# Kernel tuning notes

Hardware: AMD Instinct MI355X
Metric: run time of the kernel (lower is better)

## Reference

```python
import jax, jax.numpy as jnp
import numpy as np

B, T, H, NH = 2, 2048, 1024, 16
D = H // NH          # head dim = 64
K_CONV = 4           # short conv kernel size


def _dwconv_silu(x, w):
    # causal depthwise conv1d + silu; x:[B,T,C], w:[C,K]
    Kc = w.shape[1]
    xp = jnp.pad(x, ((0, 0), (Kc - 1, 0), (0, 0))).transpose(0, 2, 1)  # [B,C,T+K-1]
    y = jax.lax.conv_general_dilated(xp, w[:, None, :], (1,), 'VALID',
                                     feature_group_count=w.shape[0],
                                     dimension_numbers=('NCH', 'OIH', 'NCH'))
    return jax.nn.silu(y.transpose(0, 2, 1))


def _l2norm(x, eps=1e-6):
    return x * jax.lax.rsqrt(jnp.sum(x * x, -1, keepdims=True) + eps)


def _forward(hidden, Wq, Wk, Wv, conv_q, conv_k, conv_v, Wb, Wa, A_log, dt_bias, Wg, norm_w, Wo):
    Bh, Tt, Hh = hidden.shape
    nh = A_log.shape[0]
    d = Hh // nh
    q = _dwconv_silu(hidden @ Wq.T, conv_q).reshape(Bh, Tt, nh, d)
    k = _dwconv_silu(hidden @ Wk.T, conv_k).reshape(Bh, Tt, nh, d)
    v = _dwconv_silu(hidden @ Wv.T, conv_v).reshape(Bh, Tt, nh, d)
    q = _l2norm(q) * (d ** -0.5)
    k = _l2norm(k)
    beta = jax.nn.sigmoid(hidden @ Wb.T)                                  # [B,T,h]
    g = -jnp.exp(A_log) * jax.nn.softplus(hidden @ Wa.T + dt_bias)        # [B,T,h]

    def step(S, inp):
        qt, kt, vt, gt, bt = inp
        S = S * jnp.exp(gt)[..., None, None]                 # gated decay
        pred = jnp.einsum('bhk,bhkv->bhv', kt, S)            # current memory readout
        dv = (vt - pred) * bt[..., None]                     # delta-rule update
        S = S + jnp.einsum('bhk,bhv->bhkv', kt, dv)
        ot = jnp.einsum('bhk,bhkv->bhv', qt, S)
        return S, ot

    xs = (q.transpose(1, 0, 2, 3), k.transpose(1, 0, 2, 3), v.transpose(1, 0, 2, 3),
          g.transpose(1, 0, 2), beta.transpose(1, 0, 2))
    S0 = jnp.zeros((Bh, nh, d, d), hidden.dtype)
    _, o = jax.lax.scan(step, S0, xs)
    o = o.transpose(1, 0, 2, 3)                               # [B,T,h,d]
    gate = (hidden @ Wg.T).reshape(Bh, Tt, nh, d)
    o = o * jax.lax.rsqrt(jnp.mean(o * o, -1, keepdims=True) + 1e-5) * norm_w
    o = o * jax.nn.silu(gate)                                 # gated RMSNorm
    return o.reshape(Bh, Tt, Hh) @ Wo.T


def setup_inputs():
    key = jax.random.key(0)
    ks = jax.random.split(key, 16)
    s = 0.02
    return {
        'hidden': jax.random.normal(ks[0], (B, T, H), jnp.float32),
        'Wq': jax.random.normal(ks[1], (H, H), jnp.float32) * s,
        'Wk': jax.random.normal(ks[2], (H, H), jnp.float32) * s,
        'Wv': jax.random.normal(ks[3], (H, H), jnp.float32) * s,
        'conv_q': jax.random.normal(ks[4], (H, K_CONV), jnp.float32) * 0.5,
        'conv_k': jax.random.normal(ks[5], (H, K_CONV), jnp.float32) * 0.5,
        'conv_v': jax.random.normal(ks[6], (H, K_CONV), jnp.float32) * 0.5,
        'Wb': jax.random.normal(ks[7], (NH, H), jnp.float32) * s,
        'Wa': jax.random.normal(ks[8], (NH, H), jnp.float32) * s,
        'A_log': jnp.log(jax.random.uniform(ks[9], (NH,), jnp.float32, 1.0, 16.0)),
        'dt_bias': jnp.log(jnp.expm1(jax.random.uniform(ks[10], (NH,), jnp.float32, 1e-3, 0.1))),
        'Wg': jax.random.normal(ks[11], (H, H), jnp.float32) * s,
        'norm_w': jnp.ones((D,), jnp.float32),
        'Wo': jax.random.normal(ks[12], (H, H), jnp.float32) * s,
    }


def reference(hidden, Wq, Wk, Wv, conv_q, conv_k, conv_v, Wb, Wa, A_log, dt_bias, Wg, norm_w, Wo):
    return _forward(hidden, Wq, Wk, Wv, conv_q, conv_k, conv_v, Wb, Wa, A_log, dt_bias, Wg, norm_w, Wo)
```

## Files before the change

### kernel.cpp

```cpp
#include <hip/hip_runtime.h>
#include <hip/hip_bf16.h>

typedef unsigned short u16;
typedef __attribute__((ext_vector_type(4))) float f32x4;
typedef __attribute__((ext_vector_type(8))) short bf16x8;

#define TLEN 2048
#define NHEAD 16
#define HD 1024

__device__ inline u16 f2bf(float f) {
  unsigned x = __float_as_uint(f);
  return (u16)((x + 0x7fffu + ((x >> 16) & 1u)) >> 16);
}
__device__ inline float bf2f(u16 u) { return __uint_as_float(((unsigned)u) << 16); }

__device__ inline unsigned pkbf(float lo, float hi) {
  unsigned r;
  asm("v_cvt_pk_bf16_f32 %0, %1, %2" : "=v"(r) : "v"(lo), "v"(hi));
  return r;
}

__device__ inline void storev(float* p, float v) { *p = v; }
__device__ inline void storev(u16* p, float v)   { *p = f2bf(v); }

__device__ inline int rowx(int row) { return (row ^ (row >> 3)) & 7; }
__device__ inline int swz(int row, int col) {
  return (row << 7) + (((col >> 3) ^ rowx(row)) << 4) + ((col & 7) << 1);
}
__device__ inline bf16x8 frag(const u16* base, int row, int kslot) {
  return *(const bf16x8*)((const char*)base + (row << 7) +
                          ((kslot ^ rowx(row)) << 4));
}

__global__ __launch_bounds__(256) void cvt_all(
    const float* __restrict__ h,  const float* __restrict__ wq,
    const float* __restrict__ wk, const float* __restrict__ wv,
    const float* __restrict__ wg, const float* __restrict__ wo,
    const float* __restrict__ Wb, const float* __restrict__ Wa,
    u16* __restrict__ dh,  u16* __restrict__ dhlo,
    u16* __restrict__ dwq, u16* __restrict__ dwk,
    u16* __restrict__ dwv, u16* __restrict__ dwg, u16* __restrict__ dwo,
    u16* __restrict__ dwba_h, u16* __restrict__ dwba_l) {
  const int b = blockIdx.x;
  if (b < 4096) {
    const size_t i = (size_t)b * 256 + threadIdx.x;
    float4 v = *(const float4*)(h + i * 4);
    ushort4 hi, lo;
    hi.x = f2bf(v.x); lo.x = f2bf(v.x - bf2f(hi.x));
    hi.y = f2bf(v.y); lo.y = f2bf(v.y - bf2f(hi.y));
    hi.z = f2bf(v.z); lo.z = f2bf(v.z - bf2f(hi.z));
    hi.w = f2bf(v.w); lo.w = f2bf(v.w - bf2f(hi.w));
    *(ushort4*)(dh + i * 4) = hi;
    *(ushort4*)(dhlo + i * 4) = lo;
  } else if (b < 9216) {
    const int wsel = (b - 4096) >> 10;
    const size_t i = (size_t)((b - 4096) & 1023) * 256 + threadIdx.x;
    const float* s; u16* d;
    switch (wsel) {
      case 0: s = wq; d = dwq; break;
      case 1: s = wk; d = dwk; break;
      case 2: s = wv; d = dwv; break;
      case 3: s = wg; d = dwg; break;
      default: s = wo; d = dwo; break;
    }
    float4 v = *(const float4*)(s + i * 4);
    ushort4 u;
    u.x = f2bf(v.x); u.y = f2bf(v.y); u.z = f2bf(v.z); u.w = f2bf(v.w);
    *(ushort4*)(d + i * 4) = u;
  } else {
    const size_t i = (size_t)(b - 9216) * 256 + threadIdx.x;
    const size_t flat = i * 4;
    const float* src = (flat < 16384) ? (Wb + flat) : (Wa + (flat - 16384));
    float4 v = *(const float4*)src;
    ushort4 hi, lo;
    hi.x = f2bf(v.x); lo.x = f2bf(v.x - bf2f(hi.x));
    hi.y = f2bf(v.y); lo.y = f2bf(v.y - bf2f(hi.y));
    hi.z = f2bf(v.z); lo.z = f2bf(v.z - bf2f(hi.z));
    hi.w = f2bf(v.w); lo.w = f2bf(v.w - bf2f(hi.w));
    *(ushort4*)(dwba_h + flat) = hi;
    *(ushort4*)(dwba_l + flat) = lo;
  }
}

__global__ __launch_bounds__(256, 2) void gemm_big(
    const u16* __restrict__ A,
    const u16* __restrict__ W0p, const u16* __restrict__ W1p,
    const u16* __restrict__ W2p, const u16* __restrict__ W3p,
    u16* __restrict__ C0, u16* __restrict__ C1,
    u16* __restrict__ C2, u16* __restrict__ C3,
    int M, int N, int K) {
  const u16* W; u16* C;
  switch (blockIdx.z) {
    case 0: W = W0p; C = C0; break;
    case 1: W = W1p; C = C1; break;
    case 2: W = W2p; C = C2; break;
    default: W = W3p; C = C3; break;
  }
  const int tid = threadIdx.x;
  const int lane = tid & 63, wid = tid >> 6;
  const int fr = lane & 15, fq = lane >> 4;
  const int row0 = blockIdx.y * 256, col0 = blockIdx.x * 128;
  __shared__ __align__(16) u16 As[256 * 64];
  __shared__ __align__(16) u16 Bs[128 * 64];

  const u16* aSrc[8]; const u16* bSrc[4];
#pragma unroll
  for (int it = 0; it < 8; ++it) {
    const int s = it * 256 + tid;
    const int r = s >> 3, cc = s & 7;
    aSrc[it] = A + (size_t)(row0 + r) * K + (cc ^ (r & 7)) * 8;
  }
#pragma unroll
  for (int it = 0; it < 4; ++it) {
    const int s = it * 256 + tid;
    const int r = s >> 3, cc = s & 7;
    bSrc[it] = W + (size_t)(col0 + r) * K + (cc ^ (r & 7)) * 8;
  }
  int aOff[4][2], bOff[8][2];
#pragma unroll
  for (int m = 0; m < 4; ++m)
#pragma unroll
    for (int kk = 0; kk < 2; ++kk) {
      const int ra = wid * 64 + m * 16 + fr;
      aOff[m][kk] = ra * 128 + ((((kk << 2) | fq) ^ (ra & 7)) << 4);
    }
#pragma unroll
  for (int n = 0; n < 8; ++n)
#pragma unroll
    for (int kk = 0; kk < 2; ++kk) {
      const int rb = n * 16 + fr;
      bOff[n][kk] = rb * 128 + ((((kk << 2) | fq) ^ (rb & 7)) << 4);
    }

  f32x4 acc[4][8] = {};
  for (int k0 = 0; k0 < K; k0 += 64) {
#pragma unroll
    for (int it = 0; it < 8; ++it)
      __builtin_amdgcn_global_load_lds(
          (const __attribute__((address_space(1))) void*)(aSrc[it] + k0),
          (__attribute__((address_space(3))) void*)((char*)As + (it * 256 + tid) * 16),
          16, 0, 0);
#pragma unroll
    for (int it = 0; it < 4; ++it)
      __builtin_amdgcn_global_load_lds(
          (const __attribute__((address_space(1))) void*)(bSrc[it] + k0),
          (__attribute__((address_space(3))) void*)((char*)Bs + (it * 256 + tid) * 16),
          16, 0, 0);
    __syncthreads();
#pragma unroll
    for (int kk = 0; kk < 2; ++kk) {
      bf16x8 af[4], bfr[8];
#pragma unroll
      for (int m = 0; m < 4; ++m)
        af[m] = *(const bf16x8*)((const char*)As + aOff[m][kk]);
#pragma unroll
      for (int n = 0; n < 8; ++n)
        bfr[n] = *(const bf16x8*)((const char*)Bs + bOff[n][kk]);
#pragma unroll
      for (int m = 0; m < 4; ++m)
#pragma unroll
        for (int n = 0; n < 8; ++n)
          acc[m][n] = __builtin_amdgcn_mfma_f32_16x16x32_bf16(af[m], bfr[n], acc[m][n], 0, 0, 0);
    }
    __syncthreads();
  }
#pragma unroll
  for (int m = 0; m < 4; ++m)
#pragma unroll
    for (int n = 0; n < 8; ++n) {
      const int gr0 = row0 + wid * 64 + m * 16 + fq * 4;
      const int gc = col0 + n * 16 + fr;
      const unsigned c01 = pkbf(acc[m][n][0], acc[m][n][1]);
      const unsigned c23 = pkbf(acc[m][n][2], acc[m][n][3]);
      C[(size_t)(gr0 + 0) * N + gc] = (u16)c01;
      C[(size_t)(gr0 + 1) * N + gc] = (u16)(c01 >> 16);
      C[(size_t)(gr0 + 2) * N + gc] = (u16)c23;
      C[(size_t)(gr0 + 3) * N + gc] = (u16)(c23 >> 16);
    }
}

template <typename OutT, int MT>
__global__ __launch_bounds__(256) void gemm_lin(
    const u16* __restrict__ A, const u16* __restrict__ W,
    OutT* __restrict__ C, int M, int N, int K) {
  const int tid = threadIdx.x;
  const int lane = tid & 63, wid = tid >> 6;
  const int wr = wid >> 1, wc = wid & 1;
  const int fr = lane & 15, fq = lane >> 4;
  const int row0 = blockIdx.y * (MT * 32), col0 = blockIdx.x * 128;
  __shared__ __align__(16) u16 As[MT * 32 * 64];
  __shared__ __align__(16) u16 Bs[128 * 64];

  const u16* aSrc[MT]; const u16* bSrc[4];
#pragma unroll
  for (int it = 0; it < MT; ++it) {
    const int c = it * 256 + tid;
    const int r = c >> 3, cc = c & 7, sc = cc ^ (r & 7);
    aSrc[it] = A + (size_t)(row0 + r) * K + sc * 8;
  }
#pragma unroll
  for (int it = 0; it < 4; ++it) {
    const int c = it * 256 + tid;
    const int r = c >> 3, cc = c & 7, sc = cc ^ (r & 7);
    bSrc[it] = W + (size_t)(col0 + r) * K + sc * 8;
  }
  int aOff[MT][2], bOff[4][2];
#pragma unroll
  for (int m = 0; m < MT; ++m)
#pragma unroll
    for (int kk = 0; kk < 2; ++kk) {
      const int ra = wr * (MT * 16) + m * 16 + fr;
      aOff[m][kk] = ra * 128 + ((((kk << 2) | fq) ^ (fr & 7)) << 4);
    }
#pragma unroll
  for (int n = 0; n < 4; ++n)
#pragma unroll
    for (int kk = 0; kk < 2; ++kk) {
      const int rb = wc * 64 + n * 16 + fr;
      bOff[n][kk] = rb * 128 + ((((kk << 2) | fq) ^ (fr & 7)) << 4);
    }

  f32x4 acc[MT][4] = {};
  for (int k0 = 0; k0 < K; k0 += 64) {
#pragma unroll
    for (int it = 0; it < MT; ++it)
      __builtin_amdgcn_global_load_lds(
          (const __attribute__((address_space(1))) void*)(aSrc[it] + k0),
          (__attribute__((address_space(3))) void*)((char*)As + (it * 256 + wid * 64) * 16),
          16, 0, 0);
#pragma unroll
    for (int it = 0; it < 4; ++it)
      __builtin_amdgcn_global_load_lds(
          (const __attribute__((address_space(1))) void*)(bSrc[it] + k0),
          (__attribute__((address_space(3))) void*)((char*)Bs + (it * 256 + wid * 64) * 16),
          16, 0, 0);
    __syncthreads();
#pragma unroll
    for (int kk = 0; kk < 2; ++kk) {
      bf16x8 af[MT], bfr[4];
#pragma unroll
      for (int m = 0; m < MT; ++m)
        af[m] = *(const bf16x8*)((const char*)As + aOff[m][kk]);
#pragma unroll
      for (int n = 0; n < 4; ++n)
        bfr[n] = *(const bf16x8*)((const char*)Bs + bOff[n][kk]);
#pragma unroll
      for (int m = 0; m < MT; ++m)
#pragma unroll
        for (int n = 0; n < 4; ++n)
          acc[m][n] = __builtin_amdgcn_mfma_f32_16x16x32_bf16(af[m], bfr[n], acc[m][n], 0, 0, 0);
    }
    __syncthreads();
  }
#pragma unroll
  for (int m = 0; m < MT; ++m)
#pragma unroll
    for (int n = 0; n < 4; ++n)
#pragma unroll
      for (int r = 0; r < 4; ++r) {
        const int gr = row0 + wr * (MT * 16) + m * 16 + fq * 4 + r;
        const int gc = col0 + wc * 64 + n * 16 + fr;
        storev(&C[(size_t)gr * N + gc], acc[m][n][r]);
      }
}

__global__ __launch_bounds__(256) void small_mfma(
    const u16* __restrict__ hhi, const u16* __restrict__ hlo,
    const u16* __restrict__ whi, const u16* __restrict__ wlo,
    const float* __restrict__ A_log, const float* __restrict__ dtb,
    float* __restrict__ bbuf, float* __restrict__ gbuf) {
  extern __shared__ char smc[];
  u16* Ahi = (u16*)smc;
  u16* Alo = (u16*)(smc + 32768);
  float* Red = (float*)(smc + 65536);
  const int tid = threadIdx.x;
  const int row0 = blockIdx.x * 16;
#pragma unroll
  for (int i = 0; i < 8; ++i) {
    const int slot = tid + 256 * i;
    const int r = slot >> 7, s = slot & 127;
    const int ss = s ^ (r & 7);
    const size_t src = (size_t)(row0 + r) * 1024 + (size_t)ss * 8;
    __builtin_amdgcn_global_load_lds(
        (const __attribute__((address_space(1))) void*)(hhi + src),
        (__attribute__((address_space(3))) void*)(Ahi + (size_t)slot * 8), 16, 0, 0);
    __builtin_amdgcn_global_load_lds(
        (const __attribute__((address_space(1))) void*)(hlo + src),
        (__attribute__((address_space(3))) void*)(Alo + (size_t)slot * 8), 16, 0, 0);
  }
  __syncthreads();
  const int w = tid >> 6, lane = tid & 63, fr = lane & 15, fq = lane >> 4;
  f32x4 acc[2] = {};
#pragma unroll
  for (int kk = 0; kk < 8; ++kk) {
    const int s = w * 32 + kk * 4 + fq;
    const size_t k = (size_t)w * 256 + kk * 32 + fq * 8;
    const int aoff = ((fr << 7) + (s ^ (fr & 7))) * 8;
    bf16x8 ah = *(const bf16x8*)(Ahi + aoff);
    bf16x8 al = *(const bf16x8*)(Alo + aoff);
#pragma unroll
    for (int ct = 0; ct < 2; ++ct) {
      const size_t boff = (size_t)(ct * 16 + fr) * 1024 + k;
      bf16x8 bh = *(const bf16x8*)(whi + boff);
      bf16x8 bl = *(const bf16x8*)(wlo + boff);
      acc[ct] = __builtin_amdgcn_mfma_f32_16x16x32_bf16(ah, bh, acc[ct], 0, 0, 0);
      acc[ct] = __builtin_amdgcn_mfma_f32_16x16x32_bf16(ah, bl, acc[ct], 0, 0, 0);
      acc[ct] = __builtin_amdgcn_mfma_f32_16x16x32_bf16(al, bh, acc[ct], 0, 0, 0);
    }
  }
#pragma unroll
  for (int ct = 0; ct < 2; ++ct)
#pragma unroll
    for (int rr = 0; rr < 4; ++rr)
      Red[(w * 16 + fq * 4 + rr) * 33 + ct * 16 + fr] = acc[ct][rr];
  __syncthreads();
  if (tid < 128) {
    const int row = tid >> 3, cg = (tid & 7) * 4;
#pragma unroll
    for (int j = 0; j < 4; ++j) {
      const int col = cg + j;
      const float s = Red[(0 * 16 + row) * 33 + col] + Red[(1 * 16 + row) * 33 + col]
                    + Red[(2 * 16 + row) * 33 + col] + Red[(3 * 16 + row) * 33 + col];
      const int grow = row0 + row;
      if (col < 16) {
        bbuf[grow * NHEAD + col] = 1.f / (1.f + __expf(-s));
      } else {
        const int hh = col - 16;
        const float xs = s + dtb[hh];
        const float sp = (xs > 20.f) ? xs : log1pf(__expf(xs));
        gbuf[grow * NHEAD + hh] = -__expf(A_log[hh]) * sp;
      }
    }
  }
}

__global__ __launch_bounds__(256) void chunk_local(
    const u16* __restrict__ qp, const u16* __restrict__ kp, const u16* __restrict__ vp,
    const float* __restrict__ cq, const float* __restrict__ ck, const float* __restrict__ cv,
    const float* __restrict__ gbuf, const float* __restrict__ bbuf,
    u16* __restrict__ Phi, u16* __restrict__ Plo, u16* __restrict__ Ug,
    u16* __restrict__ Rg, u16* __restrict__ Yg) {
  __shared__ __align__(16) u16 Kb[64 * 64];
  __shared__ __align__(16) u16 Qb[64 * 64];
  __shared__ __align__(16) u16 K2T[64 * 64];
  __shared__ __align__(16) u16 KWt[64 * 64];
  __shared__ __align__(16) u16 Vt[64 * 64];
  __shared__ __align__(16) u16 Zb[64 * 64];
  __shared__ __align__(16) u16 Zt[64 * 64];
  __shared__ __align__(16) u16 Mb[64 * 72];
  __shared__ __align__(16) float Cb[16 * 64];
  __shared__ float bcs[64], bet[64], e2v[64], Bv[64];
  u16* WTh = Mb;
  u16* uTh = KWt;
  u16* Gb  = Vt;

  const int bid = blockIdx.x;
  const int c = bid & 31, bh = bid >> 5;
  const int b = bh >> 4, h = bh & 15;
  const int tid = threadIdx.x;

  {
    int* zp = (int*)Zt;
#pragma unroll
    for (int i = 0; i < 8; ++i) zp[tid + 256 * i] = 0;
  }
  if (tid < 64) {
    const size_t gi = (size_t)((b * TLEN + c * 64) + tid) * NHEAD + h;
    bet[tid] = bbuf[gi];
    float v = gbuf[gi];
#pragma unroll
    for (int ofs = 1; ofs < 64; ofs <<= 1) {
      float tt = __shfl_up(v, ofs);
      if (tid >= ofs) v += tt;
    }
    bcs[tid] = v;
  }
  __syncthreads();
  if (tid < 64) {
    const float blast = bcs[63];
    Bv[tid]  = __expf(bcs[tid]);
    e2v[tid] = __expf(blast - bcs[tid]);
  }
  __syncthreads();

  {
    const int dq = (tid & 15) * 4;
    const int col = h * 64 + dq;
    float4 wq4[4], wk4[4], wv4[4];
#pragma unroll
    for (int jj = 0; jj < 4; ++jj) {
      wq4[jj] = *(const float4*)(cq + (size_t)(col + jj) * 4);
      wk4[jj] = *(const float4*)(ck + (size_t)(col + jj) * 4);
      wv4[jj] = *(const float4*)(cv + (size_t)(col + jj) * 4);
    }
#pragma unroll
    for (int i = 0; i < 4; ++i) {
      const int r = i * 16 + (tid >> 4);
      const int tcur = c * 64 + r;
      ushort4 xq[4], xk[4], xv[4];
#pragma unroll
      for (int m = 0; m < 4; ++m) {
        const int tt = tcur - 3 + m;
        if (tt >= 0) {
          const size_t a = (size_t)(b * TLEN + tt) * HD + col;
          xq[m] = *(const ushort4*)(qp + a);
          xk[m] = *(const ushort4*)(kp + a);
          xv[m] = *(const ushort4*)(vp + a);
        } else {
          xq[m] = ushort4{0, 0, 0, 0}; xk[m] = xq[m]; xv[m] = xq[m];
        }
      }
      float yq[4], yk[4], yv[4];
      float ssq = 0.f, ssk = 0.f;
#pragma unroll
      for (int jj = 0; jj < 4; ++jj) {
        float aq = wq4[jj].x * bf2f(((const u16*)&xq[0])[jj]) +
                   wq4[jj].y * bf2f(((const u16*)&xq[1])[jj]) +
                   wq4[jj].z * bf2f(((const u16*)&xq[2])[jj]) +
                   wq4[jj].w * bf2f(((const u16*)&xq[3])[jj]);
        float ak = wk4[jj].x * bf2f(((const u16*)&xk[0])[jj]) +
                   wk4[jj].y * bf2f(((const u16*)&xk[1])[jj]) +
                   wk4[jj].z * bf2f(((const u16*)&xk[2])[jj]) +
                   wk4[jj].w * bf2f(((const u16*)&xk[3])[jj]);
        float av = wv4[jj].x * bf2f(((const u16*)&xv[0])[jj]) +
                   wv4[jj].y * bf2f(((const u16*)&xv[1])[jj]) +
                   wv4[jj].z * bf2f(((const u16*)&xv[2])[jj]) +
                   wv4[jj].w * bf2f(((const u16*)&xv[3])[jj]);
        yq[jj] = aq / (1.f + __expf(-aq));
        yk[jj] = ak / (1.f + __expf(-ak));
        yv[jj] = av / (1.f + __expf(-av));
        ssq += yq[jj] * yq[jj];
        ssk += yk[jj] * yk[jj];
      }
      ssq += __shfl_xor(ssq, 1); ssq += __shfl_xor(ssq, 2);
      ssq += __shfl_xor(ssq, 4); ssq += __shfl_xor(ssq, 8);
      ssk += __shfl_xor(ssk, 1); ssk += __shfl_xor(ssk, 2);
      ssk += __shfl_xor(ssk, 4); ssk += __shfl_xor(ssk, 8);
      const float qsc = rsqrtf(ssq + 1e-6f) * 0.125f;
      const float ksc = rsqrtf(ssk + 1e-6f);
      const float bR = bet[r], e2R = e2v[r], wscR = bR * Bv[r];
      float kvf[4];
#pragma unroll
      for (int jj = 0; jj < 4; ++jj) kvf[jj] = yk[jj] * ksc;
      uint2 qo2, ko2;
      qo2.x = pkbf(yq[0] * qsc, yq[1] * qsc);
      qo2.y = pkbf(yq[2] * qsc, yq[3] * qsc);
      ko2.x = pkbf(kvf[0], kvf[1]);
      ko2.y = pkbf(kvf[2], kvf[3]);
      *(uint2*)((char*)Qb + swz(r, dq)) = qo2;
      *(uint2*)((char*)Kb + swz(r, dq)) = ko2;
      const unsigned k2a = pkbf(kvf[0] * e2R, kvf[1] * e2R);
      const unsigned k2b = pkbf(kvf[2] * e2R, kvf[3] * e2R);
      const unsigned kwa = pkbf(kvf[0] * wscR, kvf[1] * wscR);
      const unsigned kwb = pkbf(kvf[2] * wscR, kvf[3] * wscR);
      const unsigned vta = pkbf(yv[0] * bR, yv[1] * bR);
      const unsigned vtb = pkbf(yv[2] * bR, yv[3] * bR);
      *(u16*)((char*)K2T + swz(dq + 0, r)) = (u16)k2a;
      *(u16*)((char*)K2T + swz(dq + 1, r)) = (u16)(k2a >> 16);
      *(u16*)((char*)K2T + swz(dq + 2, r)) = (u16)k2b;
      *(u16*)((char*)K2T + swz(dq + 3, r)) = (u16)(k2b >> 16);
      *(u16*)((char*)KWt + swz(dq + 0, r)) = (u16)kwa;
      *(u16*)((char*)KWt + swz(dq + 1, r)) = (u16)(kwa >> 16);
      *(u16*)((char*)KWt + swz(dq + 2, r)) = (u16)kwb;
      *(u16*)((char*)KWt + swz(dq + 3, r)) = (u16)(kwb >> 16);
      *(u16*)((char*)Vt + swz(dq + 0, r)) = (u16)vta;
      *(u16*)((char*)Vt + swz(dq + 1, r)) = (u16)(vta >> 16);
      *(u16*)((char*)Vt + swz(dq + 2, r)) = (u16)vtb;
      *(u16*)((char*)Vt + swz(dq + 3, r)) = (u16)(vtb >> 16);
    }
  }
  __syncthreads();

  const int w = tid >> 6, lane = tid & 63, fr = lane & 15, fq = lane >> 4;
  const int t0r = w * 16 + fq * 4;
  {
    bf16x8 ka0 = frag(Kb, w * 16 + fr, fq);
    bf16x8 ka1 = frag(Kb, w * 16 + fr, 4 + fq);
#pragma unroll
    for (int tc = 0; tc < 4; ++tc) {
      bf16x8 kb0 = frag(Kb, tc * 16 + fr, fq);
      bf16x8 kb1 = frag(Kb, tc * 16 + fr, 4 + fq);
      f32x4 a = {};
      a = __builtin_amdgcn_mfma_f32_16x16x32_bf16(ka0, kb0, a, 0, 0, 0);
      a = __builtin_amdgcn_mfma_f32_16x16x32_bf16(ka1, kb1, a, 0, 0, 0);
      const int s = tc * 16 + fr;
      float mv[4];
#pragma unroll
      for (int rr = 0; rr < 4; ++rr) {
        const int t = t0r + rr;
        mv[rr] = (s < t) ? bet[t] * __expf(bcs[t] - bcs[s]) * a[rr] : 0.f;
      }
      const unsigned m01 = pkbf(mv[0], mv[1]), m23 = pkbf(mv[2], mv[3]);
      Mb[(t0r + 0) * 72 + s] = (u16)m01;
      Mb[(t0r + 1) * 72 + s] = (u16)(m01 >> 16);
      Mb[(t0r + 2) * 72 + s] = (u16)m23;
      Mb[(t0r + 3) * 72 + s] = (u16)(m23 >> 16);
    }
  }
  __syncthreads();

#pragma unroll 1
  for (int bi = 0; bi < 4; ++bi) {
    {
      const char* mrow = (const char*)Mb + (size_t)(bi * 16 + fr) * 144;
      bf16x8 ma0 = *(const bf16x8*)(mrow + fq * 16);
      bf16x8 ma1 = *(const bf16x8*)(mrow + 64 + fq * 16);
      bf16x8 zt0 = frag(Zt, w * 16 + fr, fq);
      bf16x8 zt1 = frag(Zt, w * 16 + fr, 4 + fq);
      f32x4 a = {};
      a = __builtin_amdgcn_mfma_f32_16x16x32_bf16(ma0, zt0, a, 0, 0, 0);
      a = __builtin_amdgcn_mfma_f32_16x16x32_bf16(ma1, zt1, a, 0, 0, 0);
#pragma unroll
      for (int rr = 0; rr < 4; ++rr)
        Cb[(fq * 4 + rr) * 64 + w * 16 + fr] = a[rr];
    }
    __syncthreads();
    if (tid < 64) {
      const int j = tid;
      float z[16];
#pragma unroll
      for (int t = 0; t < 16; ++t) {
        float acc = ((bi * 16 + t) == j ? 1.f : 0.f) - Cb[t * 64 + j];
        const u16* mrow = Mb + (size_t)(bi * 16 + t) * 72 + bi * 16;
#pragma unroll
        for (int s = 0; s < t; ++s) acc -= bf2f(mrow[s]) * z[s];
        z[t] = acc;
      }
      unsigned zw[8];
#pragma unroll
      for (int t2 = 0; t2 < 8; ++t2) zw[t2] = pkbf(z[2 * t2], z[2 * t2 + 1]);
#pragma unroll
      for (int t2 = 0; t2 < 8; ++t2) {
        *(u16*)((char*)Zb + swz(bi * 16 + 2 * t2, j)) = (u16)zw[t2];
        *(u16*)((char*)Zb + swz(bi * 16 + 2 * t2 + 1, j)) = (u16)(zw[t2] >> 16);
      }
#pragma unroll
      for (int t4 = 0; t4 < 4; ++t4) {
        uint2 zz; zz.x = zw[2 * t4]; zz.y = zw[2 * t4 + 1];
        *(uint2*)((char*)Zt + swz(j, bi * 16 + t4 * 4)) = zz;
      }
    }
    __syncthreads();
  }

  f32x4 accW[4], accu[4], accG[4];
  {
    bf16x8 kw0 = frag(KWt, w * 16 + fr, fq), kw1 = frag(KWt, w * 16 + fr, 4 + fq);
    bf16x8 vt0 = frag(Vt,  w * 16 + fr, fq), vt1 = frag(Vt,  w * 16 + fr, 4 + fq);
    bf16x8 qa0 = frag(Qb,  w * 16 + fr, fq), qa1 = frag(Qb,  w * 16 + fr, 4 + fq);
#pragma unroll
    for (int tc = 0; tc < 4; ++tc) {
      bf16x8 z0 = frag(Zb, tc * 16 + fr, fq), z1 = frag(Zb, tc * 16 + fr, 4 + fq);
      bf16x8 kb0 = frag(Kb, tc * 16 + fr, fq), kb1 = frag(Kb, tc * 16 + fr, 4 + fq);
      f32x4 aw = {}, au = {}, ag = {};
      aw = __builtin_amdgcn_mfma_f32_16x16x32_bf16(kw0, z0, aw, 0, 0, 0);
      aw = __builtin_amdgcn_mfma_f32_16x16x32_bf16(kw1, z1, aw, 0, 0, 0);
      au = __builtin_amdgcn_mfma_f32_16x16x32_bf16(vt0, z0, au, 0, 0, 0);
      au = __builtin_amdgcn_mfma_f32_16x16x32_bf16(vt1, z1, au, 0, 0, 0);
      ag = __builtin_amdgcn_mfma_f32_16x16x32_bf16(qa0, kb0, ag, 0, 0, 0);
      ag = __builtin_amdgcn_mfma_f32_16x16x32_bf16(qa1, kb1, ag, 0, 0, 0);
      accW[tc] = aw; accu[tc] = au; accG[tc] = ag;
    }
  }
  __syncthreads();
#pragma unroll
  for (int tc = 0; tc < 4; ++tc) {
    const int co = tc * 16 + fr;
    const unsigned w01 = pkbf(accW[tc][0], accW[tc][1]);
    const unsigned w23 = pkbf(accW[tc][2], accW[tc][3]);
    const unsigned u01 = pkbf(accu[tc][0], accu[tc][1]);
    const unsigned u23 = pkbf(accu[tc][2], accu[tc][3]);
    float gv[4];
#pragma unroll
    for (int rr = 0; rr < 4; ++rr) {
      const int ro = t0r + rr;
      gv[rr] = (co <= ro) ? accG[tc][rr] * __expf(bcs[ro] - bcs[co]) : 0.f;
    }
    const unsigned g01 = pkbf(gv[0], gv[1]), g23 = pkbf(gv[2], gv[3]);
    *(u16*)((char*)WTh + swz(t0r + 0, co)) = (u16)w01;
    *(u16*)((char*)WTh + swz(t0r + 1, co)) = (u16)(w01 >> 16);
    *(u16*)((char*)WTh + swz(t0r + 2, co)) = (u16)w23;
    *(u16*)((char*)WTh + swz(t0r + 3, co)) = (u16)(w23 >> 16);
    *(u16*)((char*)uTh + swz(t0r + 0, co)) = (u16)u01;
    *(u16*)((char*)uTh + swz(t0r + 1, co)) = (u16)(u01 >> 16);
    *(u16*)((char*)uTh + swz(t0r + 2, co)) = (u16)u23;
    *(u16*)((char*)uTh + swz(t0r + 3, co)) = (u16)(u23 >> 16);
    *(u16*)((char*)Gb + swz(t0r + 0, co)) = (u16)g01;
    *(u16*)((char*)Gb + swz(t0r + 1, co)) = (u16)(g01 >> 16);
    *(u16*)((char*)Gb + swz(t0r + 2, co)) = (u16)g23;
    *(u16*)((char*)Gb + swz(t0r + 3, co)) = (u16)(g23 >> 16);
  }
  __syncthreads();

  {
    bf16x8 k20 = frag(K2T, w * 16 + fr, fq), k21 = frag(K2T, w * 16 + fr, 4 + fq);
    bf16x8 g0  = frag(Gb,  w * 16 + fr, fq), g1  = frag(Gb,  w * 16 + fr, 4 + fq);
    const float bl = Bv[63];
    const size_t off = (size_t)bid * 4096;
#pragma unroll
    for (int tc = 0; tc < 4; ++tc) {
      bf16x8 w0 = frag(WTh, tc * 16 + fr, fq), w1 = frag(WTh, tc * 16 + fr, 4 + fq);
      bf16x8 u0 = frag(uTh, tc * 16 + fr, fq), u1 = frag(uTh, tc * 16 + fr, 4 + fq);
      f32x4 aP = {}, aU = {}, aR = {}, aY = {};
      aP = __builtin_amdgcn_mfma_f32_16x16x32_bf16(k20, w0, aP, 0, 0, 0);
      aP = __builtin_amdgcn_mfma_f32_16x16x32_bf16(k21, w1, aP, 0, 0, 0);
      aU = __builtin_amdgcn_mfma_f32_16x16x32_bf16(k20, u0, aU, 0, 0, 0);
      aU = __builtin_amdgcn_mfma_f32_16x16x32_bf16(k21, u1, aU, 0, 0, 0);
      aR = __builtin_amdgcn_mfma_f32_16x16x32_bf16(g0, w0, aR, 0, 0, 0);
      aR = __builtin_amdgcn_mfma_f32_16x16x32_bf16(g1, w1, aR, 0, 0, 0);
      aY = __builtin_amdgcn_mfma_f32_16x16x32_bf16(g0, u0, aY, 0, 0, 0);
      aY = __builtin_amdgcn_mfma_f32_16x16x32_bf16(g1, u1, aY, 0, 0, 0);
      const int cb = tc * 16 + fr;
      float pv[4], rv[4];
#pragma unroll
      for (int rr = 0; rr < 4; ++rr) {
        const int ar = t0r + rr;
        pv[rr] = ((ar == cb) ? bl : 0.f) - aP[rr];
        const float qv = bf2f(*(const u16*)((const char*)Qb + swz(ar, cb)));
        rv[rr] = Bv[ar] * qv - aR[rr];
      }
      const unsigned p01 = pkbf(pv[0], pv[1]), p23 = pkbf(pv[2], pv[3]);
      const float l0 = pv[0] - bf2f((u16)p01), l1 = pv[1] - bf2f((u16)(p01 >> 16));
      const float l2 = pv[2] - bf2f((u16)p23), l3 = pv[3] - bf2f((u16)(p23 >> 16));
      const unsigned q01 = pkbf(l0, l1), q23 = pkbf(l2, l3);
      const unsigned u01 = pkbf(aU[0], aU[1]), u23 = pkbf(aU[2], aU[3]);
      const unsigned r01 = pkbf(rv[0], rv[1]), r23 = pkbf(rv[2], rv[3]);
      const unsigned y01 = pkbf(aY[0], aY[1]), y23 = pkbf(aY[2], aY[3]);
      const size_t o0 = off + (size_t)(t0r + 0) * 64 + cb;
      const size_t o1 = off + (size_t)(t0r + 1) * 64 + cb;
      const size_t o2 = off + (size_t)(t0r + 2) * 64 + cb;
      const size_t o3 = off + (size_t)(t0r + 3) * 64 + cb;
      Phi[o0] = (u16)p01; Phi[o1] = (u16)(p01 >> 16);
      Phi[o2] = (u16)p23; Phi[o3] = (u16)(p23 >> 16);
      Plo[o0] = (u16)q01; Plo[o1] = (u16)(q01 >> 16);
      Plo[o2] = (u16)q23; Plo[o3] = (u16)(q23 >> 16);
      Ug[o0] = (u16)u01; Ug[o1] = (u16)(u01 >> 16);
      Ug[o2] = (u16)u23; Ug[o3] = (u16)(u23 >> 16);
      Rg[o0] = (u16)r01; Rg[o1] = (u16)(r01 >> 16);
      Rg[o2] = (u16)r23; Rg[o3] = (u16)(r23 >> 16);
      Yg[o0] = (u16)y01; Yg[o1] = (u16)(y01 >> 16);
      Yg[o2] = (u16)y23; Yg[o3] = (u16)(y23 >> 16);
    }
  }
}

__global__ __launch_bounds__(256) void state_step(
    const u16* __restrict__ Phi, const u16* __restrict__ Plo,
    const u16* __restrict__ Ug, u16* __restrict__ Sst) {
  __shared__ __align__(16) u16 Sth[2][64 * 64];
  __shared__ __align__(16) u16 Stl[2][64 * 64];
  const int bh = blockIdx.x;
  const int tid = threadIdx.x;
  const int w = tid >> 6, lane = tid & 63, fr = lane & 15, fq = lane >> 4;
  const int ar0 = w * 16 + fq * 4;
  const size_t bbase = (size_t)bh * 32 * 4096;
  {
    int* p0 = (int*)&Sth[0][0];
    int* p1 = (int*)&Stl[0][0];
#pragma unroll
    for (int i = 0; i < 8; ++i) { p0[tid + 256 * i] = 0; p1[tid + 256 * i] = 0; }
    const ushort4 z4 = {0, 0, 0, 0};
#pragma unroll
    for (int i = 0; i < 4; ++i)
      *(ushort4*)(Sst + bbase + (size_t)tid * 16 + i * 4) = z4;
  }
  bf16x8 ph[2], pl[2];
  float uin[4][4];
#pragma unroll
  for (int kk = 0; kk < 2; ++kk) {
    const size_t ao = bbase + (size_t)(w * 16 + fr) * 64 + (kk * 4 + fq) * 8;
    ph[kk] = *(const bf16x8*)(Phi + ao);
    pl[kk] = *(const bf16x8*)(Plo + ao);
  }
#pragma unroll
  for (int tc = 0; tc < 4; ++tc)
#pragma unroll
    for (int rr = 0; rr < 4; ++rr)
      uin[tc][rr] = bf2f(Ug[bbase + (size_t)(ar0 + rr) * 64 + tc * 16 + fr]);
  __syncthreads();
  int cur = 0;
  for (int c = 0; c < 32; ++c) {
    f32x4 acc[4];
    bf16x8 phc[2] = {ph[0], ph[1]}, plc[2] = {pl[0], pl[1]};
#pragma unroll
    for (int tc = 0; tc < 4; ++tc)
#pragma unroll
      for (int rr = 0; rr < 4; ++rr) acc[tc][rr] = uin[tc][rr];
    if (c + 1 < 32) {
      const size_t off = bbase + (size_t)(c + 1) * 4096;
#pragma unroll
      for (int kk = 0; kk < 2; ++kk) {
        const size_t ao = off + (size_t)(w * 16 + fr) * 64 + (kk * 4 + fq) * 8;
        ph[kk] = *(const bf16x8*)(Phi + ao);
        pl[kk] = *(const bf16x8*)(Plo + ao);
      }
#pragma unroll
      for (int tc = 0; tc < 4; ++tc)
#pragma unroll
        for (int rr = 0; rr < 4; ++rr)
          uin[tc][rr] = bf2f(Ug[off + (size_t)(ar0 + rr) * 64 + tc * 16 + fr]);
    }
#pragma unroll
    for (int tc = 0; tc < 4; ++tc) {
#pragma unroll
      for (int kk = 0; kk < 2; ++kk) {
        bf16x8 sh = frag(&Sth[cur][0], tc * 16 + fr, kk * 4 + fq);
        bf16x8 sl = frag(&Stl[cur][0], tc * 16 + fr, kk * 4 + fq);
        acc[tc] = __builtin_amdgcn_mfma_f32_16x16x32_bf16(phc[kk], sh, acc[tc], 0, 0, 0);
        acc[tc] = __builtin_amdgcn_mfma_f32_16x16x32_bf16(phc[kk], sl, acc[tc], 0, 0, 0);
        acc[tc] = __builtin_amdgcn_mfma_f32_16x16x32_bf16(plc[kk], sh, acc[tc], 0, 0, 0);
      }
    }
    const int nxt = cur ^ 1;
    const size_t offn = bbase + (size_t)(c + 1) * 4096;
#pragma unroll
    for (int tc = 0; tc < 4; ++tc) {
      const int col = tc * 16 + fr;
      const unsigned h01 = pkbf(acc[tc][0], acc[tc][1]);
      const unsigned h23 = pkbf(acc[tc][2], acc[tc][3]);
      const float l0 = acc[tc][0] - bf2f((u16)h01);
      const float l1 = acc[tc][1] - bf2f((u16)(h01 >> 16));
      const float l2 = acc[tc][2] - bf2f((u16)h23);
      const float l3 = acc[tc][3] - bf2f((u16)(h23 >> 16));
      uint2 hh; hh.x = h01; hh.y = h23;
      uint2 ll; ll.x = pkbf(l0, l1); ll.y = pkbf(l2, l3);
      *(uint2*)((char*)&Sth[nxt][0] + swz(col, ar0)) = hh;
      *(uint2*)((char*)&Stl[nxt][0] + swz(col, ar0)) = ll;
      if (c + 1 < 32)
        *(uint2*)(Sst + offn + (size_t)col * 64 + ar0) = hh;
    }
    cur = nxt;
    __syncthreads();
  }
}

__global__ __launch_bounds__(256) void chunk_out(
    const u16* __restrict__ Rg, const u16* __restrict__ Yg,
    const u16* __restrict__ SstT, const u16* __restrict__ gatep,
    const float* __restrict__ norm_w, u16* __restrict__ outb) {
  const int bid = blockIdx.x;
  const int c = bid & 31, bh = bid >> 5, b = bh >> 4, h = bh & 15;
  const int tid = threadIdx.x;
  const int w = tid >> 6, lane = tid & 63, fr = lane & 15, fq = lane >> 4;
  const int ar0 = w * 16 + fq * 4;
  const size_t off = (size_t)bid * 4096;
  bf16x8 ra[2];
#pragma unroll
  for (int kk = 0; kk < 2; ++kk)
    ra[kk] = *(const bf16x8*)(Rg + off + (size_t)(w * 16 + fr) * 64 + (kk * 4 + fq) * 8);
  f32x4 acc[4];
#pragma unroll
  for (int tc = 0; tc < 4; ++tc)
#pragma unroll
    for (int rr = 0; rr < 4; ++rr)
      acc[tc][rr] = bf2f(Yg[off + (size_t)(ar0 + rr) * 64 + tc * 16 + fr]);
#pragma unroll
  for (int tc = 0; tc < 4; ++tc)
#pragma unroll
    for (int kk = 0; kk < 2; ++kk) {
      bf16x8 sb = *(const bf16x8*)(SstT + off + (size_t)(tc * 16 + fr) * 64 + (kk * 4 + fq) * 8);
      acc[tc] = __builtin_amdgcn_mfma_f32_16x16x32_bf16(ra[kk], sb, acc[tc], 0, 0, 0);
    }
  float nwv[4];
#pragma unroll
  for (int tc = 0; tc < 4; ++tc) nwv[tc] = norm_w[tc * 16 + fr];
  const size_t btbase = (size_t)(b * TLEN + c * 64);
#pragma unroll
  for (int rr = 0; rr < 4; ++rr) {
    const int t = ar0 + rr;
    float rs = acc[0][rr] * acc[0][rr] + acc[1][rr] * acc[1][rr]
             + acc[2][rr] * acc[2][rr] + acc[3][rr] * acc[3][rr];
    rs += __shfl_xor(rs, 1); rs += __shfl_xor(rs, 2);
    rs += __shfl_xor(rs, 4); rs += __shfl_xor(rs, 8);
    const float inv = rsqrtf(rs * (1.0f / 64.0f) + 1e-5f);
    const size_t rowoff = (btbase + t) * 1024 + h * 64;
#pragma unroll
    for (int tc = 0; tc < 4; ++tc) {
      const int j = tc * 16 + fr;
      const float g = bf2f(gatep[rowoff + j]);
      const float val = acc[tc][rr] * inv * nwv[tc] * (g / (1.f + __expf(-g)));
      outb[rowoff + j] = f2bf(val);
    }
  }
}

extern "C" void kernel_launch(void* const* d_in, const int* in_sizes, int n_in,
                              void* d_out, int out_size, void* d_ws, size_t ws_size,
                              hipStream_t stream) {
  const float* hidden = (const float*)d_in[0];
  const float* Wq     = (const float*)d_in[1];
  const float* Wk     = (const float*)d_in[2];
  const float* Wv     = (const float*)d_in[3];
  const float* cq     = (const float*)d_in[4];
  const float* ck     = (const float*)d_in[5];
  const float* cv     = (const float*)d_in[6];
  const float* Wb     = (const float*)d_in[7];
  const float* Wa     = (const float*)d_in[8];
  const float* A_log  = (const float*)d_in[9];
  const float* dtb    = (const float*)d_in[10];
  const float* Wg     = (const float*)d_in[11];
  const float* nw     = (const float*)d_in[12];
  const float* Wo     = (const float*)d_in[13];

  char* p = (char*)d_ws;
  const size_t MB = 1u << 20;
  u16* h_bf = (u16*)(p + 0 * MB);
  u16* wq_b = (u16*)(p + 8 * MB);
  u16* wk_b = (u16*)(p + 10 * MB);
  u16* wv_b = (u16*)(p + 12 * MB);
  u16* wg_b = (u16*)(p + 14 * MB);
  u16* Phi = (u16*)(p + 0 * MB);
  u16* Plo = (u16*)(p + 8 * MB);
  u16* wo_b = (u16*)(p + 16 * MB);
  u16* qp_b = (u16*)(p + 18 * MB);
  u16* kp_b = (u16*)(p + 26 * MB);
  u16* vp_b = (u16*)(p + 34 * MB);
  u16* gp_b = (u16*)(p + 42 * MB);
  u16*   of_b = vp_b;
  float* gbuf = (float*)(p + 50 * MB);
  float* bbuf = (float*)(p + 50 * MB + 262144);
  u16* Ug  = (u16*)(p + 51 * MB);
  u16* Rg  = (u16*)(p + 59 * MB);
  u16* Yg  = (u16*)(p + 67 * MB);
  u16* Sst = (u16*)(p + 75 * MB);
  u16* hlo_b = (u16*)(p + 83 * MB);
  u16* wba_h = (u16*)(p + 91 * MB);
  u16* wba_l = (u16*)(p + 91 * MB + 65536);

  cvt_all<<<9248, 256, 0, stream>>>(hidden, Wq, Wk, Wv, Wg, Wo, Wb, Wa,
                                    h_bf, hlo_b, wq_b, wk_b, wv_b, wg_b, wo_b,
                                    wba_h, wba_l);

  gemm_big<<<dim3(8, 16, 4), 256, 0, stream>>>(
      h_bf, wq_b, wk_b, wv_b, wg_b, qp_b, kp_b, vp_b, gp_b, 4096, 1024, 1024);

  const int sm_lds = 65536 + 8448;
  hipFuncSetAttribute((const void*)small_mfma,
                      hipFuncAttributeMaxDynamicSharedMemorySize, sm_lds);
  small_mfma<<<256, 256, sm_lds, stream>>>(h_bf, hlo_b, wba_h, wba_l,
                                           A_log, dtb, bbuf, gbuf);

  chunk_local<<<1024, 256, 0, stream>>>(qp_b, kp_b, vp_b, cq, ck, cv,
                                        gbuf, bbuf, Phi, Plo, Ug, Rg, Yg);
  state_step<<<32, 256, 0, stream>>>(Phi, Plo, Ug, Sst);
  chunk_out<<<1024, 256, 0, stream>>>(Rg, Yg, Sst, gp_b, nw, of_b);

  gemm_lin<float, 2><<<dim3(8, 64, 1), 256, 0, stream>>>(
      of_b, wo_b, (float*)d_out, 4096, 1024, 1024);
}
```

Measured before the change: 170.5 us.

## Split chunk_local work across 8 waves with 512-thread blocks

Doubles the chunk_local block from 256 to 512 threads. Each of the 8 waves now owns one 16-row tile and half of the column tiles, so per-wave MFMA and epilogue work is halved. The conv/load phase is also split over twice as many rows per iteration. The serial triangular Z solve still runs only on waves 0-3, which adds idle waves and may reduce how many blocks fit on a CU.

Measured after the change: 168.4 us. No clear change (-1.2%).

```diff
diff --git a/kernel.cpp b/kernel.cpp
--- a/kernel.cpp
+++ b/kernel.cpp
@@ -335,7 +335,7 @@
   }
 }
 
-__global__ __launch_bounds__(256) void chunk_local(
+__global__ __launch_bounds__(512) void chunk_local(
     const u16* __restrict__ qp, const u16* __restrict__ kp, const u16* __restrict__ vp,
     const float* __restrict__ cq, const float* __restrict__ ck, const float* __restrict__ cv,
     const float* __restrict__ gbuf, const float* __restrict__ bbuf,
@@ -363,7 +363,7 @@
   {
     int* zp = (int*)Zt;
 #pragma unroll
-    for (int i = 0; i < 8; ++i) zp[tid + 256 * i] = 0;
+    for (int i = 0; i < 4; ++i) zp[tid + 512 * i] = 0;
   }
   if (tid < 64) {
     const size_t gi = (size_t)((b * TLEN + c * 64) + tid) * NHEAD + h;
@@ -395,8 +395,8 @@
       wv4[jj] = *(const float4*)(cv + (size_t)(col + jj) * 4);
     }
 #pragma unroll
-    for (int i = 0; i < 4; ++i) {
-      const int r = i * 16 + (tid >> 4);
+    for (int i = 0; i < 2; ++i) {
+      const int r = i * 32 + (tid >> 4);
       const int tcur = c * 64 + r;
       ushort4 xq[4], xk[4], xv[4];
 #pragma unroll
@@ -473,12 +473,15 @@
   __syncthreads();
 
   const int w = tid >> 6, lane = tid & 63, fr = lane & 15, fq = lane >> 4;
-  const int t0r = w * 16 + fq * 4;
+  const int wr = w >> 1;
+  const int tc0 = (w & 1) * 2;
+  const int t0r = wr * 16 + fq * 4;
   {
-    bf16x8 ka0 = frag(Kb, w * 16 + fr, fq);
-    bf16x8 ka1 = frag(Kb, w * 16 + fr, 4 + fq);
-#pragma unroll
-    for (int tc = 0; tc < 4; ++tc) {
+    bf16x8 ka0 = frag(Kb, wr * 16 + fr, fq);
+    bf16x8 ka1 = frag(Kb, wr * 16 + fr, 4 + fq);
+#pragma unroll
+    for (int j = 0; j < 2; ++j) {
+      const int tc = tc0 + j;
       bf16x8 kb0 = frag(Kb, tc * 16 + fr, fq);
       bf16x8 kb1 = frag(Kb, tc * 16 + fr, 4 + fq);
       f32x4 a = {};
@@ -502,7 +505,7 @@
 
 #pragma unroll 1
   for (int bi = 0; bi < 4; ++bi) {
-    {
+    if (w < 4) {
       const char* mrow = (const char*)Mb + (size_t)(bi * 16 + fr) * 144;
       bf16x8 ma0 = *(const bf16x8*)(mrow + fq * 16);
       bf16x8 ma1 = *(const bf16x8*)(mrow + 64 + fq * 16);
@@ -544,13 +547,14 @@
     __syncthreads();
   }
 
-  f32x4 accW[4], accu[4], accG[4];
+  f32x4 accW[2], accu[2], accG[2];
   {
-    bf16x8 kw0 = frag(KWt, w * 16 + fr, fq), kw1 = frag(KWt, w * 16 + fr, 4 + fq);
-    bf16x8 vt0 = frag(Vt,  w * 16 + fr, fq), vt1 = frag(Vt,  w * 16 + fr, 4 + fq);
-    bf16x8 qa0 = frag(Qb,  w * 16 + fr, fq), qa1 = frag(Qb,  w * 16 + fr, 4 + fq);
-#pragma unroll
-    for (int tc = 0; tc < 4; ++tc) {
+    bf16x8 kw0 = frag(KWt, wr * 16 + fr, fq), kw1 = frag(KWt, wr * 16 + fr, 4 + fq);
+    bf16x8 vt0 = frag(Vt,  wr * 16 + fr, fq), vt1 = frag(Vt,  wr * 16 + fr, 4 + fq);
+    bf16x8 qa0 = frag(Qb,  wr * 16 + fr, fq), qa1 = frag(Qb,  wr * 16 + fr, 4 + fq);
+#pragma unroll
+    for (int j = 0; j < 2; ++j) {
+      const int tc = tc0 + j;
       bf16x8 z0 = frag(Zb, tc * 16 + fr, fq), z1 = frag(Zb, tc * 16 + fr, 4 + fq);
       bf16x8 kb0 = frag(Kb, tc * 16 + fr, fq), kb1 = frag(Kb, tc * 16 + fr, 4 + fq);
       f32x4 aw = {}, au = {}, ag = {};
@@ -560,22 +564,23 @@
       au = __builtin_amdgcn_mfma_f32_16x16x32_bf16(vt1, z1, au, 0, 0, 0);
       ag = __builtin_amdgcn_mfma_f32_16x16x32_bf16(qa0, kb0, ag, 0, 0, 0);
       ag = __builtin_amdgcn_mfma_f32_16x16x32_bf16(qa1, kb1, ag, 0, 0, 0);
-      accW[tc] = aw; accu[tc] = au; accG[tc] = ag;
+      accW[j] = aw; accu[j] = au; accG[j] = ag;
     }
   }
   __syncthreads();
 #pragma unroll
-  for (int tc = 0; tc < 4; ++tc) {
+  for (int j = 0; j < 2; ++j) {
+    const int tc = tc0 + j;
     const int co = tc * 16 + fr;
-    const unsigned w01 = pkbf(accW[tc][0], accW[tc][1]);
-    const unsigned w23 = pkbf(accW[tc][2], accW[tc][3]);
-    const unsigned u01 = pkbf(accu[tc][0], accu[tc][1]);
-    const unsigned u23 = pkbf(accu[tc][2], accu[tc][3]);
+    const unsigned w01 = pkbf(accW[j][0], accW[j][1]);
+    const unsigned w23 = pkbf(accW[j][2], accW[j][3]);
+    const unsigned u01 = pkbf(accu[j][0], accu[j][1]);
+    const unsigned u23 = pkbf(accu[j][2], accu[j][3]);
     float gv[4];
 #pragma unroll
     for (int rr = 0; rr < 4; ++rr) {
       const int ro = t0r + rr;
-      gv[rr] = (co <= ro) ? accG[tc][rr] * __expf(bcs[ro] - bcs[co]) : 0.f;
+      gv[rr] = (co <= ro) ? accG[j][rr] * __expf(bcs[ro] - bcs[co]) : 0.f;
     }
     const unsigned g01 = pkbf(gv[0], gv[1]), g23 = pkbf(gv[2], gv[3]);
     *(u16*)((char*)WTh + swz(t0r + 0, co)) = (u16)w01;
@@ -594,12 +599,13 @@
   __syncthreads();
 
   {
-    bf16x8 k20 = frag(K2T, w * 16 + fr, fq), k21 = frag(K2T, w * 16 + fr, 4 + fq);
-    bf16x8 g0  = frag(Gb,  w * 16 + fr, fq), g1  = frag(Gb,  w * 16 + fr, 4 + fq);
+    bf16x8 k20 = frag(K2T, wr * 16 + fr, fq), k21 = frag(K2T, wr * 16 + fr, 4 + fq);
+    bf16x8 g0  = frag(Gb,  wr * 16 + fr, fq), g1  = frag(Gb,  wr * 16 + fr, 4 + fq);
     const float bl = Bv[63];
     const size_t off = (size_t)bid * 4096;
 #pragma unroll
-    for (int tc = 0; tc < 4; ++tc) {
+    for (int j = 0; j < 2; ++j) {
+      const int tc = tc0 + j;
       bf16x8 w0 = frag(WTh, tc * 16 + fr, fq), w1 = frag(WTh, tc * 16 + fr, 4 + fq);
       bf16x8 u0 = frag(uTh, tc * 16 + fr, fq), u1 = frag(uTh, tc * 16 + fr, 4 + fq);
       f32x4 aP = {}, aU = {}, aR = {}, aY = {};
@@ -841,7 +847,7 @@
   small_mfma<<<256, 256, sm_lds, stream>>>(h_bf, hlo_b, wba_h, wba_l,
                                            A_log, dtb, bbuf, gbuf);
 
-  chunk_local<<<1024, 256, 0, stream>>>(qp_b, kp_b, vp_b, cq, ck, cv,
+  chunk_local<<<1024, 512, 0, stream>>>(qp_b, kp_b, vp_b, cq, ck, cv,
                                         gbuf, bbuf, Phi, Plo, Ug, Rg, Yg);
   state_step<<<32, 256, 0, stream>>>(Phi, Plo, Ug, Sst);
   chunk_out<<<1024, 256, 0, stream>>>(Rg, Yg, Sst, gp_b, nw, of_b);
```
